# Optimization experiments

Measured on AMD Instinct MI355X. Metric: run time of the kernel, lower is better.

Reference implementation:

```python
import jax, jax.numpy as jnp
import numpy as np

N_EXPERTS = 8
TOPK = 2
D_MODEL = 1024
D_FF = 4096

def setup_inputs() -> dict:
    key = jax.random.key(0)
    k_x, k_g, k_1, k_2 = jax.random.split(key, 4)
    x = jax.random.normal(k_x, (4, 2048, D_MODEL), dtype=jnp.float32)
    Wg = jax.random.normal(k_g, (D_MODEL, N_EXPERTS), dtype=jnp.float32) * 0.02
    W1 = jax.random.normal(k_1, (N_EXPERTS, D_MODEL, D_FF), dtype=jnp.float32) * 0.02
    W2 = jax.random.normal(k_2, (N_EXPERTS, D_FF, D_MODEL), dtype=jnp.float32) * 0.02
    return {"x": x, "Wg": Wg, "W1": W1, "W2": W2}

def reference(x, Wg, W1, W2):
    B, S, D = x.shape
    xt = x.reshape(-1, D)                      # [T, D]
    T = xt.shape[0]
    logits = xt @ Wg                            # [T, E]
    vals, idx = jax.lax.top_k(logits, TOPK)     # [T, K]
    w = jax.nn.softmax(vals, axis=-1)           # renormalize over selected experts
    # scatter top-k weights into dense [T, E] gate matrix (zeros elsewhere)
    gates = jnp.zeros((T, N_EXPERTS), dtype=x.dtype).at[jnp.arange(T)[:, None], idx].set(w)
    out = jnp.zeros_like(xt)
    for e in range(N_EXPERTS):                  # fixed small loop over experts
        h = jax.nn.silu(xt @ W1[e]) @ W2[e]     # [T, D]
        out = out + gates[:, e:e+1] * h
    return out.reshape(B, S, D)
```

## Files before the change

kernel.cpp:

```cpp
#include <hip/hip_runtime.h>
#include <hip/hip_bf16.h>
#include <math.h>

#define T_TOK 8192
#define DM 1024
#define DF 4096
#define NE 8
#define MAXT 72

typedef __attribute__((ext_vector_type(4))) float  f32x4;
typedef __attribute__((ext_vector_type(8))) short  s16x8;
typedef __attribute__((ext_vector_type(8))) unsigned short u16x8;

__device__ __forceinline__ unsigned short f2bf(float f) {
    unsigned int u = __builtin_bit_cast(unsigned int, f);
    u = (u + 0x7FFFu + ((u >> 16) & 1u)) >> 16;
    return (unsigned short)u;
}

#define GLDS16(gptr, lptr)                                                         \
    __builtin_amdgcn_global_load_lds(                                              \
        (const __attribute__((address_space(1))) void*)(gptr),                     \
        (__attribute__((address_space(3))) void*)(lptr), 16, 0, 0)

#define BAR() asm volatile("s_barrier" ::: "memory")

template<int W>
__device__ __forceinline__ void waitvm() {
    if constexpr (W == 3)      asm volatile("s_waitcnt vmcnt(3)" ::: "memory");
    else                       asm volatile("s_waitcnt vmcnt(0)" ::: "memory");
}

__global__ __launch_bounds__(256) void route_kernel(
    const float* __restrict__ x, const float* __restrict__ Wg,
    int* __restrict__ counts, int* __restrict__ lists, float* __restrict__ pw)
{
    int tok  = (int)((blockIdx.x * blockDim.x + threadIdx.x) >> 6);
    int lane = threadIdx.x & 63;
    if (tok >= T_TOK) return;

    const float* xr = x + (size_t)tok * DM;
    float acc[NE];
#pragma unroll
    for (int e = 0; e < NE; ++e) acc[e] = 0.f;

    for (int i = lane; i < DM; i += 64) {
        float xv = xr[i];
        const float* wr = Wg + (size_t)i * NE;
#pragma unroll
        for (int e = 0; e < NE; ++e) acc[e] += xv * wr[e];
    }
#pragma unroll
    for (int e = 0; e < NE; ++e) {
#pragma unroll
        for (int off = 32; off > 0; off >>= 1)
            acc[e] += __shfl_xor(acc[e], off, 64);
    }

    if (lane == 0) {
        int i0 = 0; float v0 = acc[0];
#pragma unroll
        for (int e = 1; e < NE; ++e) if (acc[e] > v0) { v0 = acc[e]; i0 = e; }
        int i1 = -1; float v1 = -INFINITY;
#pragma unroll
        for (int e = 0; e < NE; ++e) if (e != i0 && acc[e] > v1) { v1 = acc[e]; i1 = e; }
        float e1 = __expf(v1 - v0);
        float s  = 1.f + e1;
        int p0 = tok * 2, p1 = tok * 2 + 1;
        pw[p0] = 1.f / s;
        pw[p1] = e1 / s;
        int pos0 = atomicAdd(&counts[i0], 1);
        lists[i0 * T_TOK + pos0] = p0;
        int pos1 = atomicAdd(&counts[i1], 1);
        lists[i1 * T_TOK + pos1] = p1;
    }
}

__global__ void offsets_kernel(const int* __restrict__ counts, int* __restrict__ offsets,
                               unsigned* __restrict__ table, int* __restrict__ ntp)
{
    if (threadIdx.x == 0) {
        int s = 0, ti = 0;
        for (int e = 0; e < NE; ++e) {
            offsets[e] = s;
            int cnt = counts[e];
            for (int t0 = 0; t0 < cnt; t0 += 256)
                table[ti++] = ((unsigned)e << 20) | (unsigned)t0;
            s += cnt;
        }
        ntp[0] = ti;
        for (; ti < MAXT; ++ti) table[ti] = 0xFFFFFFFFu;
    }
}

__global__ __launch_bounds__(256) void conv_x_kernel(
    const float* __restrict__ x, unsigned short* __restrict__ xb)
{
    size_t i = ((size_t)blockIdx.x * 256 + threadIdx.x) * 8;
    float4 v0 = *reinterpret_cast<const float4*>(x + i);
    float4 v1 = *reinterpret_cast<const float4*>(x + i + 4);
    u16x8 o;
    o[0] = f2bf(v0.x); o[1] = f2bf(v0.y); o[2] = f2bf(v0.z); o[3] = f2bf(v0.w);
    o[4] = f2bf(v1.x); o[5] = f2bf(v1.y); o[6] = f2bf(v1.z); o[7] = f2bf(v1.w);
    *reinterpret_cast<u16x8*>(xb + i) = o;
}

template<int K, int N>
__global__ __launch_bounds__(256) void transpose_conv_kernel(
    const float* __restrict__ W, unsigned short* __restrict__ Wt)
{
    int e  = blockIdx.z;
    int k0 = blockIdx.x * 64;
    int n0 = blockIdx.y * 64;
    const float* We = W + (size_t)e * K * N;
    unsigned short* Wte = Wt + (size_t)e * K * N;

    __shared__ unsigned short t[64][73];
    int c4 = (threadIdx.x & 15) * 4;
    int r  = threadIdx.x >> 4;
#pragma unroll
    for (int i = 0; i < 4; ++i) {
        int rr = r + i * 16;
        float4 v = *reinterpret_cast<const float4*>(We + (size_t)(k0 + rr) * N + n0 + c4);
        t[rr][c4 + 0] = f2bf(v.x); t[rr][c4 + 1] = f2bf(v.y);
        t[rr][c4 + 2] = f2bf(v.z); t[rr][c4 + 3] = f2bf(v.w);
    }
    __syncthreads();
    int kc = (threadIdx.x & 7) * 8;
    int rn = threadIdx.x >> 3;
#pragma unroll
    for (int i = 0; i < 2; ++i) {
        int nn = rn + i * 32;
        u16x8 o;
#pragma unroll
        for (int j = 0; j < 8; ++j) o[j] = t[kc + j][nn];
        *reinterpret_cast<u16x8*>(Wte + (size_t)(n0 + nn) * K + k0 + kc) = o;
    }
}

template<int N, int K, int SPLITK, bool IS_G1>
__global__ __launch_bounds__(512, 4) void moe_gemm7(
    const unsigned short* __restrict__ A,
    const unsigned short* __restrict__ Wt,
    const int* __restrict__ counts, const int* __restrict__ offsets,
    const int* __restrict__ lists, const unsigned* __restrict__ table,
    const int* __restrict__ ntp, const float* __restrict__ pw,
    unsigned short* __restrict__ Hout, float* __restrict__ Oout)
{
    constexpr int NT  = N / 128;
    constexpr int PAN = NT * SPLITK;
    constexpr int KS  = K / SPLITK;
    constexpr int NC  = KS / 32;
    static_assert(NC >= 4, "pipeline depth");

    __shared__ __attribute__((aligned(16))) char lds[49152];

    int ntl  = ntp[0];
    int live = ntl * PAN;
    int orig = blockIdx.x;
    if (orig >= live) return;
    int q = live >> 3, r = live & 7;
    int xq = orig & 7, ib = orig >> 3;
    int work = (xq < r ? xq * (q + 1) : r * (q + 1) + (xq - r) * q) + ib;
    int rt    = work / PAN;
    int panel = work - rt * PAN;
    int nt    = panel >> (SPLITK - 1);
    int sk    = panel & (SPLITK - 1);
    int koff  = sk * KS;

    unsigned te = table[rt];
    int e     = (int)(te >> 20);
    int slot0 = (int)(te & 0xFFFFFu);
    int cnt   = counts[e];
    int off   = offsets[e];
    int ntile = nt * 128;

    int tid  = threadIdx.x;
    int lane = tid & 63;
    int wid  = tid >> 6;
    int wm = wid >> 1;
    int wn = wid & 1;
    int l15 = lane & 15, l4 = lane >> 4;

    const unsigned short* Be = Wt + (size_t)e * N * K;

    int ssw = ((tid & 3) ^ ((tid >> 3) & 3)) * 8;
    unsigned aOff0, aOff1, bOff;
    {
        int r0 = tid >> 2;
#pragma unroll
        for (int u = 0; u < 2; ++u) {
            int sl = slot0 + u * 128 + r0;
            unsigned grow;
            if (IS_G1) grow = (sl < cnt) ? (unsigned)(lists[e * T_TOK + sl] >> 1) : 0u;
            else       grow = (unsigned)(off + ((sl < cnt) ? sl : slot0));
            unsigned v = grow * (unsigned)K + (unsigned)(koff + ssw);
            if (u == 0) aOff0 = v; else aOff1 = v;
        }
        bOff = (unsigned)(ntile + r0) * (unsigned)K + (unsigned)(koff + ssw);
    }

    auto stage = [&](int s, int c) {
        int ko = c * 32;
        char* dA = lds + s * 16384 + tid * 16;
        char* dB = lds + 32768 + s * 8192 + tid * 16;
        GLDS16(A + aOff0 + ko, dA);
        GLDS16(A + aOff1 + ko, dA + 8192);
        GLDS16(Be + bOff + ko, dB);
    };

    int swzb = (l4 ^ ((l15 >> 1) & 3)) * 16;
    int aRd = (wm * 64 + l15) * 64 + swzb;
    int bRd = (wn * 64 + l15) * 64 + swzb;

    f32x4 acc[4][4];
#pragma unroll
    for (int m = 0; m < 4; ++m)
#pragma unroll
        for (int n = 0; n < 4; ++n) acc[m][n] = (f32x4){0.f, 0.f, 0.f, 0.f};

    auto compute = [&](int s) {
        const char* Ab = lds + s * 16384;
        const char* Bb = lds + 32768 + s * 8192;
        s16x8 af[4];
#pragma unroll
        for (int m = 0; m < 4; ++m)
            af[m] = *reinterpret_cast<const s16x8*>(Ab + aRd + m * 1024);
        __builtin_amdgcn_s_setprio(1);
#pragma unroll
        for (int n = 0; n < 4; ++n) {
            s16x8 bf = *reinterpret_cast<const s16x8*>(Bb + bRd + n * 1024);
#pragma unroll
            for (int m = 0; m < 4; ++m)
                acc[m][n] = __builtin_amdgcn_mfma_f32_16x16x32_bf16(af[m], bf, acc[m][n], 0, 0, 0);
        }
        __builtin_amdgcn_s_setprio(0);
    };

    stage(0, 0); stage(1, 1);
    for (int c = 0; c < NC - 2; ++c) {
        waitvm<3>(); BAR();
        compute(c & 1);
        BAR();
        stage(c & 1, c + 2);
    }
    waitvm<3>(); BAR(); compute(0); BAR();
    waitvm<0>(); BAR(); compute(1);

#pragma unroll
    for (int m = 0; m < 4; ++m) {
        int trow = wm * 64 + m * 16 + l4 * 4;
#pragma unroll
        for (int rr = 0; rr < 4; ++rr) {
            int slot = slot0 + trow + rr;
            if (slot >= cnt) continue;
            if (IS_G1) {
                unsigned short* hr = Hout + (size_t)(off + slot) * N;
#pragma unroll
                for (int n = 0; n < 4; ++n) {
                    int col = ntile + wn * 64 + n * 16 + l15;
                    float v = acc[m][n][rr];
                    float s = v / (1.f + __expf(-v));
                    hr[col] = f2bf(s);
                }
            } else {
                int p = lists[e * T_TOK + slot];
                float w = pw[p];
                float* orow = Oout + (size_t)(p >> 1) * DM;
#pragma unroll
                for (int n = 0; n < 4; ++n) {
                    int col = ntile + wn * 64 + n * 16 + l15;
                    atomicAdd(orow + col, w * acc[m][n][rr]);
                }
            }
        }
    }
}

#define BMF 16
#define BFF 256
__global__ __launch_bounds__(256) void expert_gemm_f32(
    const float* __restrict__ x, const float* __restrict__ W1, const float* __restrict__ W2,
    const int* __restrict__ counts, const int* __restrict__ lists, const float* __restrict__ pw,
    float* __restrict__ out)
{
    int e    = blockIdx.y;
    int tile = blockIdx.x;
    int cnt  = counts[e];
    int start = tile * BMF;
    if (start >= cnt) return;

    __shared__ float xs[BMF][DM];
    __shared__ float hs[BMF][BFF];
    __shared__ int   toks[BMF];
    __shared__ float wgt[BMF];

    int tid = threadIdx.x;
    int nm  = cnt - start; if (nm > BMF) nm = BMF;

    if (tid < BMF) {
        if (tid < nm) {
            int p = lists[e * T_TOK + start + tid];
            toks[tid] = p >> 1;
            wgt[tid]  = pw[p];
        } else { toks[tid] = -1; wgt[tid] = 0.f; }
    }
    __syncthreads();
    for (int m = 0; m < BMF; ++m) {
        int t = toks[m];
        const float* xr = (t >= 0) ? (x + (size_t)t * DM) : nullptr;
        for (int i = tid; i < DM; i += 256) xs[m][i] = (t >= 0) ? xr[i] : 0.f;
    }
    __syncthreads();

    const float* W1e = W1 + (size_t)e * DM * DF;
    const float* W2e = W2 + (size_t)e * DF * DM;
    float acc[BMF][4];
#pragma unroll
    for (int m = 0; m < BMF; ++m)
#pragma unroll
        for (int c = 0; c < 4; ++c) acc[m][c] = 0.f;

    for (int fc = 0; fc < DF; fc += BFF) {
        float hacc[BMF];
#pragma unroll
        for (int m = 0; m < BMF; ++m) hacc[m] = 0.f;
        const float* w1col = W1e + fc + tid;
#pragma unroll 4
        for (int i = 0; i < DM; ++i) {
            float w1v = w1col[(size_t)i * DF];
#pragma unroll
            for (int m = 0; m < BMF; ++m) hacc[m] += xs[m][i] * w1v;
        }
        __syncthreads();
#pragma unroll
        for (int m = 0; m < BMF; ++m) {
            float v = hacc[m];
            hs[m][tid] = v / (1.f + __expf(-v));
        }
        __syncthreads();
        const float* w2base = W2e + (size_t)fc * DM + tid * 4;
        for (int f = 0; f < BFF; ++f) {
            float4 w2v = *reinterpret_cast<const float4*>(w2base + (size_t)f * DM);
#pragma unroll
            for (int m = 0; m < BMF; ++m) {
                float h = hs[m][f];
                acc[m][0] += h * w2v.x; acc[m][1] += h * w2v.y;
                acc[m][2] += h * w2v.z; acc[m][3] += h * w2v.w;
            }
        }
        __syncthreads();
    }
    int c0 = tid * 4;
#pragma unroll
    for (int m = 0; m < BMF; ++m) {
        int t = toks[m];
        if (t < 0) continue;
        float w = wgt[m];
        float* op = out + (size_t)t * DM + c0;
        atomicAdd(op + 0, w * acc[m][0]);
        atomicAdd(op + 1, w * acc[m][1]);
        atomicAdd(op + 2, w * acc[m][2]);
        atomicAdd(op + 3, w * acc[m][3]);
    }
}

extern "C" void kernel_launch(void* const* d_in, const int* in_sizes, int n_in,
                              void* d_out, int out_size, void* d_ws, size_t ws_size,
                              hipStream_t stream)
{
    const float* x  = (const float*)d_in[0];
    const float* Wg = (const float*)d_in[1];
    const float* W1 = (const float*)d_in[2];
    const float* W2 = (const float*)d_in[3];
    float* out = (float*)d_out;

    char* ws = (char*)d_ws;
    int*      counts  = (int*)(ws + 0);
    int*      offsets = (int*)(ws + 64);
    int*      ntp     = (int*)(ws + 128);
    unsigned* table   = (unsigned*)(ws + 256);
    int*      lists   = (int*)(ws + 2048);
    float*    pw      = (float*)(ws + 2048 + 262144);

    const size_t o_xb  = 524288;
    const size_t sz_xb = (size_t)T_TOK * DM * 2;
    const size_t o_w1t = o_xb + sz_xb;
    const size_t sz_w  = (size_t)NE * DM * DF * 2;
    const size_t o_w2t = o_w1t + sz_w;
    const size_t o_h   = o_w2t + sz_w;
    const size_t sz_h  = (size_t)(2 * T_TOK) * DF * 2;
    const size_t NEEDED = o_h + sz_h;

    hipMemsetAsync(counts, 0, 64, stream);
    route_kernel<<<T_TOK / 4, 256, 0, stream>>>(x, Wg, counts, lists, pw);

    if (ws_size >= NEEDED) {
        unsigned short* xb  = (unsigned short*)(ws + o_xb);
        unsigned short* w1t = (unsigned short*)(ws + o_w1t);
        unsigned short* w2t = (unsigned short*)(ws + o_w2t);
        unsigned short* H   = (unsigned short*)(ws + o_h);

        hipMemsetAsync(d_out, 0, (size_t)out_size * sizeof(float), stream);
        offsets_kernel<<<1, 64, 0, stream>>>(counts, offsets, table, ntp);
        conv_x_kernel<<<(T_TOK * DM) / (256 * 8), 256, 0, stream>>>(x, xb);
        {
            dim3 g(DM / 64, DF / 64, NE);
            transpose_conv_kernel<DM, DF><<<g, 256, 0, stream>>>(W1, w1t);
        }
        {
            dim3 g(DF / 64, DM / 64, NE);
            transpose_conv_kernel<DF, DM><<<g, 256, 0, stream>>>(W2, w2t);
        }
        moe_gemm7<DF, DM, 1, true><<<dim3(MAXT * 32), 512, 0, stream>>>(
            xb, w1t, counts, offsets, lists, table, ntp, pw, H, nullptr);
        moe_gemm7<DM, DF, 2, false><<<dim3(MAXT * 16), 512, 0, stream>>>(
            H, w2t, counts, offsets, lists, table, ntp, pw, nullptr, out);
    } else {
        hipMemsetAsync(d_out, 0, (size_t)out_size * sizeof(float), stream);
        dim3 grid(T_TOK / BMF, NE);
        expert_gemm_f32<<<grid, 256, 0, stream>>>(x, W1, W2, counts, lists, pw, out);
    }
}
```

Before: 712.8 us.

## Enlarge MoE GEMM tiles to 256x256 with 64-wide K stages

```diff
diff --git a/kernel.cpp b/kernel.cpp
--- a/kernel.cpp
+++ b/kernel.cpp
@@ -27,7 +27,7 @@
 
 template<int W>
 __device__ __forceinline__ void waitvm() {
-    if constexpr (W == 3)      asm volatile("s_waitcnt vmcnt(3)" ::: "memory");
+    if constexpr (W == 8)      asm volatile("s_waitcnt vmcnt(8)" ::: "memory");
     else                       asm volatile("s_waitcnt vmcnt(0)" ::: "memory");
 }
 
@@ -139,7 +139,7 @@
 }
 
 template<int N, int K, int SPLITK, bool IS_G1>
-__global__ __launch_bounds__(512, 4) void moe_gemm7(
+__global__ __launch_bounds__(512, 2) void moe_gemm8(
     const unsigned short* __restrict__ A,
     const unsigned short* __restrict__ Wt,
     const int* __restrict__ counts, const int* __restrict__ offsets,
@@ -147,13 +147,13 @@
     const int* __restrict__ ntp, const float* __restrict__ pw,
     unsigned short* __restrict__ Hout, float* __restrict__ Oout)
 {
-    constexpr int NT  = N / 128;
+    constexpr int NT  = N / 256;
     constexpr int PAN = NT * SPLITK;
     constexpr int KS  = K / SPLITK;
-    constexpr int NC  = KS / 32;
-    static_assert(NC >= 4, "pipeline depth");
-
-    __shared__ __attribute__((aligned(16))) char lds[49152];
+    constexpr int NKT = KS / 64;
+    static_assert(NKT >= 2, "pipeline depth");
+
+    __shared__ __attribute__((aligned(16))) char lds[131072];
 
     int ntl  = ntp[0];
     int live = ntl * PAN;
@@ -164,8 +164,8 @@
     int work = (xq < r ? xq * (q + 1) : r * (q + 1) + (xq - r) * q) + ib;
     int rt    = work / PAN;
     int panel = work - rt * PAN;
-    int nt    = panel >> (SPLITK - 1);
-    int sk    = panel & (SPLITK - 1);
+    int nt    = (SPLITK == 2) ? (panel >> 1) : panel;
+    int sk    = (SPLITK == 2) ? (panel & 1) : 0;
     int koff  = sk * KS;
 
     unsigned te = table[rt];
@@ -173,83 +173,108 @@
     int slot0 = (int)(te & 0xFFFFFu);
     int cnt   = counts[e];
     int off   = offsets[e];
-    int ntile = nt * 128;
+    int ntile = nt * 256;
 
     int tid  = threadIdx.x;
     int lane = tid & 63;
     int wid  = tid >> 6;
-    int wm = wid >> 1;
-    int wn = wid & 1;
+    int wm = wid >> 2;
+    int wn = wid & 3;
     int l15 = lane & 15, l4 = lane >> 4;
 
     const unsigned short* Be = Wt + (size_t)e * N * K;
 
-    int ssw = ((tid & 3) ^ ((tid >> 3) & 3)) * 8;
-    unsigned aOff0, aOff1, bOff;
+    int ssw = ((tid & 7) ^ ((tid >> 3) & 7)) * 8;
+    int r0  = tid >> 3;
+    unsigned aOff0, aOff1, aOff2, aOff3;
     {
-        int r0 = tid >> 2;
-#pragma unroll
-        for (int u = 0; u < 2; ++u) {
-            int sl = slot0 + u * 128 + r0;
+#pragma unroll
+        for (int u = 0; u < 4; ++u) {
+            int sl = slot0 + u * 64 + r0;
             unsigned grow;
             if (IS_G1) grow = (sl < cnt) ? (unsigned)(lists[e * T_TOK + sl] >> 1) : 0u;
             else       grow = (unsigned)(off + ((sl < cnt) ? sl : slot0));
             unsigned v = grow * (unsigned)K + (unsigned)(koff + ssw);
-            if (u == 0) aOff0 = v; else aOff1 = v;
-        }
-        bOff = (unsigned)(ntile + r0) * (unsigned)K + (unsigned)(koff + ssw);
-    }
-
-    auto stage = [&](int s, int c) {
-        int ko = c * 32;
-        char* dA = lds + s * 16384 + tid * 16;
-        char* dB = lds + 32768 + s * 8192 + tid * 16;
+            if (u == 0) aOff0 = v; else if (u == 1) aOff1 = v;
+            else if (u == 2) aOff2 = v; else aOff3 = v;
+        }
+    }
+    unsigned bOff0 = (unsigned)(ntile + 0   + r0) * (unsigned)K + (unsigned)(koff + ssw);
+    unsigned bOff1 = (unsigned)(ntile + 64  + r0) * (unsigned)K + (unsigned)(koff + ssw);
+    unsigned bOff2 = (unsigned)(ntile + 128 + r0) * (unsigned)K + (unsigned)(koff + ssw);
+    unsigned bOff3 = (unsigned)(ntile + 192 + r0) * (unsigned)K + (unsigned)(koff + ssw);
+
+    auto stage = [&](int s, int kt) {
+        int ko = kt * 64;
+        char* dA = lds + s * 32768 + tid * 16;
+        char* dB = lds + 65536 + s * 32768 + tid * 16;
         GLDS16(A + aOff0 + ko, dA);
         GLDS16(A + aOff1 + ko, dA + 8192);
-        GLDS16(Be + bOff + ko, dB);
+        GLDS16(A + aOff2 + ko, dA + 16384);
+        GLDS16(A + aOff3 + ko, dA + 24576);
+        GLDS16(Be + bOff0 + ko, dB);
+        GLDS16(Be + bOff1 + ko, dB + 8192);
+        GLDS16(Be + bOff2 + ko, dB + 16384);
+        GLDS16(Be + bOff3 + ko, dB + 24576);
     };
 
-    int swzb = (l4 ^ ((l15 >> 1) & 3)) * 16;
-    int aRd = (wm * 64 + l15) * 64 + swzb;
-    int bRd = (wn * 64 + l15) * 64 + swzb;
-
-    f32x4 acc[4][4];
-#pragma unroll
-    for (int m = 0; m < 4; ++m)
+    int swz  = (l4 ^ (l15 & 7)) * 16;
+    int aRdB = (wm * 128 + l15) * 128 + swz;
+    int bRdB = (wn * 64  + l15) * 128 + swz;
+
+    f32x4 acc[8][4];
+#pragma unroll
+    for (int m = 0; m < 8; ++m)
 #pragma unroll
         for (int n = 0; n < 4; ++n) acc[m][n] = (f32x4){0.f, 0.f, 0.f, 0.f};
 
-    auto compute = [&](int s) {
-        const char* Ab = lds + s * 16384;
-        const char* Bb = lds + 32768 + s * 8192;
-        s16x8 af[4];
-#pragma unroll
-        for (int m = 0; m < 4; ++m)
-            af[m] = *reinterpret_cast<const s16x8*>(Ab + aRd + m * 1024);
-        __builtin_amdgcn_s_setprio(1);
-#pragma unroll
-        for (int n = 0; n < 4; ++n) {
-            s16x8 bf = *reinterpret_cast<const s16x8*>(Bb + bRd + n * 1024);
-#pragma unroll
-            for (int m = 0; m < 4; ++m)
-                acc[m][n] = __builtin_amdgcn_mfma_f32_16x16x32_bf16(af[m], bf, acc[m][n], 0, 0, 0);
-        }
-        __builtin_amdgcn_s_setprio(0);
+    auto tilestep = [&](int s) {
+        const char* Ab = lds + s * 32768;
+        const char* Bb = lds + 65536 + s * 32768;
+#pragma unroll
+        for (int kh = 0; kh < 2; ++kh) {
+            const int khx = kh * 64;
+            s16x8 bf[4];
+#pragma unroll
+            for (int n = 0; n < 4; ++n)
+                bf[n] = *reinterpret_cast<const s16x8*>(Bb + ((bRdB + n * 2048) ^ khx));
+#pragma unroll
+            for (int mh = 0; mh < 2; ++mh) {
+                s16x8 af[4];
+#pragma unroll
+                for (int m = 0; m < 4; ++m)
+                    af[m] = *reinterpret_cast<const s16x8*>(Ab + ((aRdB + (mh * 4 + m) * 2048) ^ khx));
+                __builtin_amdgcn_s_setprio(1);
+#pragma unroll
+                for (int n = 0; n < 4; ++n)
+#pragma unroll
+                    for (int m = 0; m < 4; ++m)
+                        acc[mh * 4 + m][n] = __builtin_amdgcn_mfma_f32_16x16x32_bf16(
+                            af[m], bf[n], acc[mh * 4 + m][n], 0, 0, 0);
+                __builtin_amdgcn_s_setprio(0);
+                BAR();
+            }
+        }
     };
 
-    stage(0, 0); stage(1, 1);
-    for (int c = 0; c < NC - 2; ++c) {
-        waitvm<3>(); BAR();
-        compute(c & 1);
+    stage(0, 0);
+    stage(1, 1);
+    waitvm<8>();
+    BAR();
+    for (int kt = 0; kt < NKT; ++kt) {
+        tilestep(kt & 1);
+        if (kt + 2 < NKT) {
+            stage(kt & 1, kt + 2);
+            waitvm<8>();
+        } else {
+            waitvm<0>();
+        }
         BAR();
-        stage(c & 1, c + 2);
-    }
-    waitvm<3>(); BAR(); compute(0); BAR();
-    waitvm<0>(); BAR(); compute(1);
-
-#pragma unroll
-    for (int m = 0; m < 4; ++m) {
-        int trow = wm * 64 + m * 16 + l4 * 4;
+    }
+
+#pragma unroll
+    for (int m = 0; m < 8; ++m) {
+        int trow = wm * 128 + m * 16 + l4 * 4;
 #pragma unroll
         for (int rr = 0; rr < 4; ++rr) {
             int slot = slot0 + trow + rr;
@@ -412,9 +437,9 @@
             dim3 g(DF / 64, DM / 64, NE);
             transpose_conv_kernel<DF, DM><<<g, 256, 0, stream>>>(W2, w2t);
         }
-        moe_gemm7<DF, DM, 1, true><<<dim3(MAXT * 32), 512, 0, stream>>>(
+        moe_gemm8<DF, DM, 1, true><<<dim3(MAXT * (DF / 256)), 512, 0, stream>>>(
             xb, w1t, counts, offsets, lists, table, ntp, pw, H, nullptr);
-        moe_gemm7<DM, DF, 2, false><<<dim3(MAXT * 16), 512, 0, stream>>>(
+        moe_gemm8<DM, DF, 2, false><<<dim3(MAXT * (DM / 256) * 2), 512, 0, stream>>>(
             H, w2t, counts, offsets, lists, table, ntp, pw, nullptr, out);
     } else {
         hipMemsetAsync(d_out, 0, (size_t)out_size * sizeof(float), stream);
```

Result: slower. 810.2 us (+13.7%).

## Triple-buffer MoE GEMM LDS pipeline and fuse x bf16 conversion into routing

Applied to the files above, without the earlier changes.

```diff
diff --git a/kernel.cpp b/kernel.cpp
--- a/kernel.cpp
+++ b/kernel.cpp
@@ -11,6 +11,7 @@
 typedef __attribute__((ext_vector_type(4))) float  f32x4;
 typedef __attribute__((ext_vector_type(8))) short  s16x8;
 typedef __attribute__((ext_vector_type(8))) unsigned short u16x8;
+typedef __attribute__((ext_vector_type(4))) unsigned short u16x4;
 
 __device__ __forceinline__ unsigned short f2bf(float f) {
     unsigned int u = __builtin_bit_cast(unsigned int, f);
@@ -27,13 +28,15 @@
 
 template<int W>
 __device__ __forceinline__ void waitvm() {
-    if constexpr (W == 3)      asm volatile("s_waitcnt vmcnt(3)" ::: "memory");
+    if constexpr (W == 6)      asm volatile("s_waitcnt vmcnt(6)" ::: "memory");
+    else if constexpr (W == 3) asm volatile("s_waitcnt vmcnt(3)" ::: "memory");
     else                       asm volatile("s_waitcnt vmcnt(0)" ::: "memory");
 }
 
 __global__ __launch_bounds__(256) void route_kernel(
     const float* __restrict__ x, const float* __restrict__ Wg,
-    int* __restrict__ counts, int* __restrict__ lists, float* __restrict__ pw)
+    int* __restrict__ counts, int* __restrict__ lists, float* __restrict__ pw,
+    unsigned short* __restrict__ xb)
 {
     int tok  = (int)((blockIdx.x * blockDim.x + threadIdx.x) >> 6);
     int lane = threadIdx.x & 63;
@@ -50,6 +53,18 @@
 #pragma unroll
         for (int e = 0; e < NE; ++e) acc[e] += xv * wr[e];
     }
+
+    if (xb) {
+        unsigned short* xrow = xb + (size_t)tok * DM;
+#pragma unroll
+        for (int i = lane * 4; i < DM; i += 256) {
+            float4 v = *reinterpret_cast<const float4*>(xr + i);
+            u16x4 o;
+            o[0] = f2bf(v.x); o[1] = f2bf(v.y); o[2] = f2bf(v.z); o[3] = f2bf(v.w);
+            *reinterpret_cast<u16x4*>(xrow + i) = o;
+        }
+    }
+
 #pragma unroll
     for (int e = 0; e < NE; ++e) {
 #pragma unroll
@@ -93,18 +108,6 @@
     }
 }
 
-__global__ __launch_bounds__(256) void conv_x_kernel(
-    const float* __restrict__ x, unsigned short* __restrict__ xb)
-{
-    size_t i = ((size_t)blockIdx.x * 256 + threadIdx.x) * 8;
-    float4 v0 = *reinterpret_cast<const float4*>(x + i);
-    float4 v1 = *reinterpret_cast<const float4*>(x + i + 4);
-    u16x8 o;
-    o[0] = f2bf(v0.x); o[1] = f2bf(v0.y); o[2] = f2bf(v0.z); o[3] = f2bf(v0.w);
-    o[4] = f2bf(v1.x); o[5] = f2bf(v1.y); o[6] = f2bf(v1.z); o[7] = f2bf(v1.w);
-    *reinterpret_cast<u16x8*>(xb + i) = o;
-}
-
 template<int K, int N>
 __global__ __launch_bounds__(256) void transpose_conv_kernel(
     const float* __restrict__ W, unsigned short* __restrict__ Wt)
@@ -139,7 +142,7 @@
 }
 
 template<int N, int K, int SPLITK, bool IS_G1>
-__global__ __launch_bounds__(512, 4) void moe_gemm7(
+__global__ __launch_bounds__(512, 4) void moe_gemm11(
     const unsigned short* __restrict__ A,
     const unsigned short* __restrict__ Wt,
     const int* __restrict__ counts, const int* __restrict__ offsets,
@@ -153,7 +156,7 @@
     constexpr int NC  = KS / 32;
     static_assert(NC >= 4, "pipeline depth");
 
-    __shared__ __attribute__((aligned(16))) char lds[49152];
+    __shared__ __attribute__((aligned(16))) char lds[73728];
 
     int ntl  = ntp[0];
     int live = ntl * PAN;
@@ -203,7 +206,7 @@
     auto stage = [&](int s, int c) {
         int ko = c * 32;
         char* dA = lds + s * 16384 + tid * 16;
-        char* dB = lds + 32768 + s * 8192 + tid * 16;
+        char* dB = lds + 49152 + s * 8192 + tid * 16;
         GLDS16(A + aOff0 + ko, dA);
         GLDS16(A + aOff1 + ko, dA + 8192);
         GLDS16(Be + bOff + ko, dB);
@@ -221,7 +224,7 @@
 
     auto compute = [&](int s) {
         const char* Ab = lds + s * 16384;
-        const char* Bb = lds + 32768 + s * 8192;
+        const char* Bb = lds + 49152 + s * 8192;
         s16x8 af[4];
 #pragma unroll
         for (int m = 0; m < 4; ++m)
@@ -237,15 +240,18 @@
         __builtin_amdgcn_s_setprio(0);
     };
 
-    stage(0, 0); stage(1, 1);
-    for (int c = 0; c < NC - 2; ++c) {
-        waitvm<3>(); BAR();
-        compute(c & 1);
+    stage(0, 0); stage(1, 1); stage(2, 2);
+    int sslot = 0;
+    for (int c = 0; c < NC; ++c) {
+        if (c + 2 < NC)      waitvm<6>();
+        else if (c + 1 < NC) waitvm<3>();
+        else                 waitvm<0>();
         BAR();
-        stage(c & 1, c + 2);
-    }
-    waitvm<3>(); BAR(); compute(0); BAR();
-    waitvm<0>(); BAR(); compute(1);
+        compute(sslot);
+        BAR();
+        if (c + 3 < NC) stage(sslot, c + 3);
+        sslot = (sslot == 2) ? 0 : sslot + 1;
+    }
 
 #pragma unroll
     for (int m = 0; m < 4; ++m) {
@@ -392,18 +398,19 @@
     const size_t sz_h  = (size_t)(2 * T_TOK) * DF * 2;
     const size_t NEEDED = o_h + sz_h;
 
+    bool fast = (ws_size >= NEEDED);
+    unsigned short* xb = fast ? (unsigned short*)(ws + o_xb) : nullptr;
+
     hipMemsetAsync(counts, 0, 64, stream);
-    route_kernel<<<T_TOK / 4, 256, 0, stream>>>(x, Wg, counts, lists, pw);
-
-    if (ws_size >= NEEDED) {
-        unsigned short* xb  = (unsigned short*)(ws + o_xb);
+    route_kernel<<<T_TOK / 4, 256, 0, stream>>>(x, Wg, counts, lists, pw, xb);
+
+    if (fast) {
         unsigned short* w1t = (unsigned short*)(ws + o_w1t);
         unsigned short* w2t = (unsigned short*)(ws + o_w2t);
         unsigned short* H   = (unsigned short*)(ws + o_h);
 
         hipMemsetAsync(d_out, 0, (size_t)out_size * sizeof(float), stream);
         offsets_kernel<<<1, 64, 0, stream>>>(counts, offsets, table, ntp);
-        conv_x_kernel<<<(T_TOK * DM) / (256 * 8), 256, 0, stream>>>(x, xb);
         {
             dim3 g(DM / 64, DF / 64, NE);
             transpose_conv_kernel<DM, DF><<<g, 256, 0, stream>>>(W1, w1t);
@@ -412,9 +419,9 @@
             dim3 g(DF / 64, DM / 64, NE);
             transpose_conv_kernel<DF, DM><<<g, 256, 0, stream>>>(W2, w2t);
         }
-        moe_gemm7<DF, DM, 1, true><<<dim3(MAXT * 32), 512, 0, stream>>>(
+        moe_gemm11<DF, DM, 1, true><<<dim3(MAXT * 32), 512, 0, stream>>>(
             xb, w1t, counts, offsets, lists, table, ntp, pw, H, nullptr);
-        moe_gemm7<DM, DF, 2, false><<<dim3(MAXT * 16), 512, 0, stream>>>(
+        moe_gemm11<DM, DF, 2, false><<<dim3(MAXT * 16), 512, 0, stream>>>(
             H, w2t, counts, offsets, lists, table, ntp, pw, nullptr, out);
     } else {
         hipMemsetAsync(d_out, 0, (size_t)out_size * sizeof(float), stream);
```

Result: faster. 695.3 us (-2.5%).
